# Kernel optimization log

Hardware: AMD Instinct MI355X
Metric: run time of the kernel (lower is better)

The kernel has to match this reference:

```python
import jax, jax.numpy as jnp
import numpy as np

F_IN = 512
F_OUT = 512
HEADS = 8  # all heads share the same weights in the original module
NEG_SLOPE = 0.01  # nn.LeakyReLU default
MASK_VAL = -1.0e10


def setup_inputs() -> dict:
    key = jax.random.key(0)
    ks = jax.random.split(key, 6)
    B, N = 8, 2048
    X_input = jax.random.normal(ks[0], (B, N, F_IN), dtype=jnp.float32)
    u = jax.random.uniform(ks[1], (B, N, N), dtype=jnp.float32)
    A_input = jnp.maximum((u < 0.02).astype(jnp.float32), jnp.eye(N, dtype=jnp.float32)[None])
    # learned params (nn.Linear stores W as [out,in]; we use [in,out] with x @ W)
    Wk = jax.random.normal(ks[2], (F_IN, F_OUT), dtype=jnp.float32) / np.sqrt(F_IN).astype(np.float32)
    bk = jnp.zeros((F_OUT,), dtype=jnp.float32)
    ws = jax.random.normal(ks[3], (F_OUT,), dtype=jnp.float32) / np.sqrt(F_OUT).astype(np.float32)
    bs = jnp.zeros((), dtype=jnp.float32)
    wn = jax.random.normal(ks[4], (F_OUT,), dtype=jnp.float32) / np.sqrt(F_OUT).astype(np.float32)
    bn = jnp.zeros((), dtype=jnp.float32)
    return {"X_input": X_input, "A_input": A_input, "Wk": Wk, "bk": bk,
            "ws": ws, "bs": bs, "wn": wn, "bn": bn}


def reference(X_input, A_input, Wk, bk, ws, bs, wn, bn):
    # shared projection (identical across all heads in the original loop)
    feat = jnp.einsum('bnf,fg->bng', X_input, Wk) + bk          # [B,N,F_]
    a_self = jnp.einsum('bng,g->bn', feat, ws) + bs             # [B,N]
    a_neigh = jnp.einsum('bng,g->bn', feat, wn) + bn            # [B,N]
    # torch.bmm([B,N,1],[B,1,N]) -> multiplicative outer product score
    att = jax.nn.leaky_relu(a_self[:, :, None] * a_neigh[:, None, :], NEG_SLOPE)
    att = att + MASK_VAL * (1.0 - A_input)                      # [B,N,N]
    p = jax.nn.softmax(att, axis=-1)
    nf = jnp.einsum('bij,bjg->big', p, feat)                    # [B,N,F_]
    # concat of HEADS identical head outputs, then tanh
    out = jnp.tanh(jnp.concatenate([nf] * HEADS, axis=-1))      # [B,N,HEADS*F_]
    return out
```

## Files before the change

kernel.cpp:

```cpp
#include <hip/hip_runtime.h>

#define NEG_SLOPE 0.01f
#define B_ 8
#define N_ 2048
#define F_ 512

typedef unsigned short u16;
typedef __attribute__((ext_vector_type(8))) unsigned short u16x8;
typedef __attribute__((ext_vector_type(8))) _Float16 f16x8;
typedef __attribute__((ext_vector_type(4))) float f32x4;

__device__ __forceinline__ f32x4 mfma16f(u16x8 a, u16x8 b, f32x4 c) {
    return __builtin_amdgcn_mfma_f32_16x16x32_f16(
        __builtin_bit_cast(f16x8, a), __builtin_bit_cast(f16x8, b), c, 0, 0, 0);
}

__device__ __forceinline__ void load_lds16(const void* g, void* l) {
    __builtin_amdgcn_global_load_lds(
        (__attribute__((address_space(1))) void*)(void*)g,
        (__attribute__((address_space(3))) void*)l, 16, 0, 0);
}

__global__ __launch_bounds__(256) void prep_all(const float* __restrict__ Wk,
                                                const float* __restrict__ bk,
                                                const float* __restrict__ ws,
                                                const float* __restrict__ bs,
                                                const float* __restrict__ wn,
                                                const float* __restrict__ bn,
                                                u16* __restrict__ Wf,
                                                float* __restrict__ ws2,
                                                float* __restrict__ wn2,
                                                float* __restrict__ csn) {
    const int bid = blockIdx.x, t = threadIdx.x;
    if (bid < 1024) {
        const int id = bid * 256 + t;
        const int k = id & 511, n = id >> 9;
        ((_Float16*)Wf)[id] = (_Float16)Wk[k * 512 + n];
        return;
    }
    const int lane = t & 63, w = t >> 6;
    if (bid >= 1280) {
        if (w == 0) {
            const int sel = bid - 1280;
            const float* vec = sel ? wn : ws;
            const float4 b0 = *(const float4*)(bk + lane * 8);
            const float4 b1 = *(const float4*)(bk + lane * 8 + 4);
            const float4 v0 = *(const float4*)(vec + lane * 8);
            const float4 v1 = *(const float4*)(vec + lane * 8 + 4);
            float d = b0.x * v0.x + b0.y * v0.y + b0.z * v0.z + b0.w * v0.w +
                      b1.x * v1.x + b1.y * v1.y + b1.z * v1.z + b1.w * v1.w;
#pragma unroll
            for (int m = 32; m; m >>= 1) d += __shfl_xor(d, m);
            if (lane == 0) csn[sel] = d + (sel ? bn[0] : bs[0]);
        }
        return;
    }
    const int W = (bid - 1024) * 4 + w;
    const int k = W & 511;
    const float* vec = (W < 512) ? ws : wn;
    const float4 w0 = *(const float4*)(Wk + (size_t)k * 512 + lane * 8);
    const float4 w1 = *(const float4*)(Wk + (size_t)k * 512 + lane * 8 + 4);
    const float4 v0 = *(const float4*)(vec + lane * 8);
    const float4 v1 = *(const float4*)(vec + lane * 8 + 4);
    float d = w0.x * v0.x + w0.y * v0.y + w0.z * v0.z + w0.w * v0.w +
              w1.x * v1.x + w1.y * v1.y + w1.z * v1.z + w1.w * v1.w;
#pragma unroll
    for (int m = 32; m; m >>= 1) d += __shfl_xor(d, m);
    if (lane == 0) ((W < 512) ? ws2 : wn2)[k] = d;
}

__global__ __launch_bounds__(256) void gemm_feat(const float* __restrict__ X,
                                                 const u16* __restrict__ Wf,
                                                 const float* __restrict__ bk,
                                                 u16* __restrict__ feat) {
    __shared__ u16 Af[128 * 64];
    __shared__ u16 Bf[128 * 64];
    const int t = threadIdx.x;
    const int lane = t & 63;
    const int w = t >> 6;
    const int bid = blockIdx.x;
    const int tm = (bid & 7) * 16 + (bid >> 5);
    const int tn = (bid >> 3) & 3;
    const int wr = w >> 1, wc = w & 1;

    f32x4 acc[4][4];
#pragma unroll
    for (int m = 0; m < 4; ++m)
#pragma unroll
        for (int n = 0; n < 4; ++n) acc[m][n] = {0.f, 0.f, 0.f, 0.f};

    const int lrow = lane >> 3;
    const int scol = ((lane & 7) ^ lrow) * 8;
    const u16* Bbase = Wf + ((size_t)(tn * 128 + w * 8 + lrow)) * 512 + scol;
    u16* BfW = Bf + (w * 8) * 64;

    const int arow = t >> 3;
    const int akk = (t & 7) * 8;
    const float* Abase = X + ((size_t)(tm * 128 + arow)) * 512 + akk;
    u16* AfW = Af + arow * 64 + (akk ^ ((arow & 7) * 8));

    for (int k0 = 0; k0 < 512; k0 += 64) {
#pragma unroll
        for (int iss = 0; iss < 4; ++iss)
            load_lds16(Bbase + (size_t)(iss * 32) * 512 + k0, BfW + iss * 32 * 64);
#pragma unroll
        for (int p = 0; p < 4; ++p) {
            const float4 x0 = *(const float4*)(Abase + (size_t)(p * 32) * 512 + k0);
            const float4 x1 = *(const float4*)(Abase + (size_t)(p * 32) * 512 + k0 + 4);
            const float xv[8] = {x0.x, x0.y, x0.z, x0.w, x1.x, x1.y, x1.z, x1.w};
            u16x8 hv;
#pragma unroll
            for (int e = 0; e < 8; ++e)
                hv[e] = __builtin_bit_cast(u16, (_Float16)xv[e]);
            *(u16x8*)(AfW + p * 32 * 64) = hv;
        }
        __syncthreads();
        const int swz = (lane & 7) * 8;
#pragma unroll
        for (int kk = 0; kk < 64; kk += 32) {
            u16x8 af[4], bf[4];
            const int aoff = (kk + (lane >> 4) * 8) ^ swz;
#pragma unroll
            for (int m = 0; m < 4; ++m)
                af[m] = *(const u16x8*)(Af + (wr * 64 + m * 16 + (lane & 15)) * 64 + aoff);
#pragma unroll
            for (int n = 0; n < 4; ++n)
                bf[n] = *(const u16x8*)(Bf + (wc * 64 + n * 16 + (lane & 15)) * 64 + aoff);
#pragma unroll
            for (int m = 0; m < 4; ++m)
#pragma unroll
                for (int n = 0; n < 4; ++n)
                    acc[m][n] = mfma16f(af[m], bf[n], acc[m][n]);
        }
        __syncthreads();
    }

    const int crow0 = tm * 128 + wr * 64;
    const int ccol0 = tn * 128 + wc * 64;
    _Float16* feat16 = (_Float16*)feat;
#pragma unroll
    for (int n = 0; n < 4; ++n) {
        const int gc = ccol0 + n * 16 + (lane & 15);
        const float bkv = bk[gc];
#pragma unroll
        for (int m = 0; m < 4; ++m) {
            const int gr = crow0 + m * 16 + (lane >> 4) * 4;
#pragma unroll
            for (int r = 0; r < 4; ++r)
                feat16[(size_t)(gr + r) * 512 + gc] = (_Float16)(acc[m][n][r] + bkv);
        }
    }
}

__global__ __launch_bounds__(256) void dots_x(const float* __restrict__ X,
                                              const float* __restrict__ ws2,
                                              const float* __restrict__ wn2,
                                              const float* __restrict__ csn,
                                              float* __restrict__ a_self,
                                              float* __restrict__ a_neigh) {
    const int t = threadIdx.x, lane = t & 63, w = t >> 6;
    const int row = blockIdx.x * 4 + w;
    const float4 f0 = *(const float4*)(X + (size_t)row * 512 + lane * 8);
    const float4 f1 = *(const float4*)(X + (size_t)row * 512 + lane * 8 + 4);
    const float fv[8] = {f0.x, f0.y, f0.z, f0.w, f1.x, f1.y, f1.z, f1.w};
    const float4 sa = *(const float4*)(ws2 + lane * 8);
    const float4 sb = *(const float4*)(ws2 + lane * 8 + 4);
    const float4 na = *(const float4*)(wn2 + lane * 8);
    const float4 nb = *(const float4*)(wn2 + lane * 8 + 4);
    float ds = fv[0] * sa.x + fv[1] * sa.y + fv[2] * sa.z + fv[3] * sa.w +
               fv[4] * sb.x + fv[5] * sb.y + fv[6] * sb.z + fv[7] * sb.w;
    float dn = fv[0] * na.x + fv[1] * na.y + fv[2] * na.z + fv[3] * na.w +
               fv[4] * nb.x + fv[5] * nb.y + fv[6] * nb.z + fv[7] * nb.w;
#pragma unroll
    for (int m = 32; m; m >>= 1) {
        ds += __shfl_xor(ds, m);
        dn += __shfl_xor(dn, m);
    }
    if (lane == 0) {
        a_self[row] = ds + csn[0];
        a_neigh[row] = dn + csn[1];
    }
}

__global__ __launch_bounds__(256) void attn_row(const float* __restrict__ A,
                                                const u16* __restrict__ feat,
                                                const float* __restrict__ a_self,
                                                const float* __restrict__ a_neigh,
                                                float* __restrict__ out) {
    const int bid = blockIdx.x;
    const int row = (bid & 7) * N_ + (bid >> 3);
    const int b = bid & 7;
    const int t = threadIdx.x;
    const int lane = t & 63, w = t >> 6;

    __shared__ u16   lj[N_];
    __shared__ float lsv[N_];
    __shared__ int   wtot[4];
    __shared__ float wred[8];
    __shared__ float nfw[4][F_];

    const float asi = a_self[row];

    const float4* Arow = (const float4*)(A + (size_t)row * N_);
    const float4* An   = (const float4*)(a_neigh + b * N_);
    const float4 a0 = Arow[t * 2], a1 = Arow[t * 2 + 1];
    const float4 n0 = An[t * 2],   n1 = An[t * 2 + 1];
    const float av[8] = {a0.x, a0.y, a0.z, a0.w, a1.x, a1.y, a1.z, a1.w};
    const float nv[8] = {n0.x, n0.y, n0.z, n0.w, n1.x, n1.y, n1.z, n1.w};
    float sv[8];
    int cnt = 0;
    float mloc = -3.0e38f;
#pragma unroll
    for (int e = 0; e < 8; ++e) {
        float s = asi * nv[e];
        s = s > 0.f ? s : NEG_SLOPE * s;
        sv[e] = s;
        if (av[e] != 0.f) { ++cnt; mloc = fmaxf(mloc, s); }
    }
    int v = cnt;
#pragma unroll
    for (int off = 1; off < 64; off <<= 1) {
        const int u = __shfl_up(v, off);
        if (lane >= off) v += u;
    }
#pragma unroll
    for (int m = 32; m; m >>= 1) mloc = fmaxf(mloc, __shfl_xor(mloc, m));
    if (lane == 63) wtot[w] = v;
    if (lane == 0) wred[w] = mloc;
    __syncthreads();
    int base = v - cnt;
#pragma unroll
    for (int i = 0; i < 4; ++i) base += (i < w) ? wtot[i] : 0;
    const int total = wtot[0] + wtot[1] + wtot[2] + wtot[3];
    const float mx = fmaxf(fmaxf(wred[0], wred[1]), fmaxf(wred[2], wred[3]));

    float ssum = 0.f;
    int pos = base;
#pragma unroll
    for (int e = 0; e < 8; ++e) {
        if (av[e] != 0.f) {
            const float wv = __expf(sv[e] - mx);
            lj[pos] = (u16)(t * 8 + e);
            lsv[pos] = wv;
            ssum += wv;
            ++pos;
        }
    }
#pragma unroll
    for (int m = 32; m; m >>= 1) ssum += __shfl_xor(ssum, m);
    if (lane == 0) wred[4 + w] = ssum;
    __syncthreads();
    const float inv = 1.f / (wred[4] + wred[5] + wred[6] + wred[7]);

    const u16* frow = feat + (size_t)b * N_ * F_ + lane * 8;
    float acc[8] = {0.f, 0.f, 0.f, 0.f, 0.f, 0.f, 0.f, 0.f};
    int k = w;
    for (; k + 4 < total; k += 8) {
        const size_t j0 = (size_t)lj[k] * F_, j1 = (size_t)lj[k + 4] * F_;
        const float p0 = lsv[k], p1 = lsv[k + 4];
        const f16x8 v0 = *(const f16x8*)(frow + j0);
        const f16x8 v1 = *(const f16x8*)(frow + j1);
#pragma unroll
        for (int e = 0; e < 8; ++e) acc[e] += p0 * (float)v0[e] + p1 * (float)v1[e];
    }
    if (k < total) {
        const size_t j0 = (size_t)lj[k] * F_;
        const float p0 = lsv[k];
        const f16x8 v0 = *(const f16x8*)(frow + j0);
#pragma unroll
        for (int e = 0; e < 8; ++e) acc[e] += p0 * (float)v0[e];
    }
#pragma unroll
    for (int e = 0; e < 8; ++e) nfw[w][lane * 8 + e] = acc[e];
    __syncthreads();

    const int f0 = t * 2;
    const float nf0 = (nfw[0][f0] + nfw[1][f0]) + (nfw[2][f0] + nfw[3][f0]);
    const float nf1 = (nfw[0][f0 + 1] + nfw[1][f0 + 1]) + (nfw[2][f0 + 1] + nfw[3][f0 + 1]);
    const float o0 = tanhf(nf0 * inv);
    const float o1 = tanhf(nf1 * inv);
    const float2 o = make_float2(o0, o1);
    float* obase = out + (size_t)row * (8 * F_) + f0;
#pragma unroll
    for (int h = 0; h < 8; ++h) *(float2*)(obase + h * F_) = o;
}

extern "C" void kernel_launch(void* const* d_in, const int* in_sizes, int n_in,
                              void* d_out, int out_size, void* d_ws, size_t ws_size,
                              hipStream_t stream) {
    const float* X  = (const float*)d_in[0];
    const float* A  = (const float*)d_in[1];
    const float* Wk = (const float*)d_in[2];
    const float* bk = (const float*)d_in[3];
    const float* ws = (const float*)d_in[4];
    const float* bs = (const float*)d_in[5];
    const float* wn = (const float*)d_in[6];
    const float* bn = (const float*)d_in[7];
    float* out = (float*)d_out;

    char* wsb = (char*)d_ws;
    u16*   feat    = (u16*)(wsb);
    u16*   Wf      = (u16*)(wsb + 16777216);
    float* a_self  = (float*)(wsb + 17301504);
    float* a_neigh = (float*)(wsb + 17367040);
    float* ws2     = (float*)(wsb + 17432576);
    float* wn2     = (float*)(wsb + 17434624);
    float* csn     = (float*)(wsb + 17436672);

    prep_all   <<<dim3(1282),  dim3(256), 0, stream>>>(Wk, bk, ws, bs, wn, bn, Wf, ws2, wn2, csn);
    gemm_feat  <<<dim3(512),   dim3(256), 0, stream>>>(X, Wf, bk, feat);
    dots_x     <<<dim3(4096),  dim3(256), 0, stream>>>(X, ws2, wn2, csn, a_self, a_neigh);
    attn_row   <<<dim3(16384), dim3(256), 0, stream>>>(A, feat, a_self, a_neigh, out);
}
```

Measured before the change: 146.2 us.

## Process one attention row per wavefront using ballot-driven sparse gather

Restructures attn_row so each 64-lane wave owns a whole row instead of a 256-thread block splitting one row. The nonzero adjacency entries are tracked in per-lane bitmasks, then walked with ballot/ctz while scores are broadcast by shuffle. This drops the LDS compaction, prefix scan, cross-wave reductions and all __syncthreads, and the grid shrinks to a quarter of the blocks. The cost is that the gather over neighbors is now serial within one wave, with no two-way unrolling and more exp evaluations per lane. It also swaps the launch order of dots_x and gemm_feat, which are independent.

```diff
diff --git a/kernel.cpp b/kernel.cpp
--- a/kernel.cpp
+++ b/kernel.cpp
@@ -188,101 +188,70 @@
                                                 const float* __restrict__ a_neigh,
                                                 float* __restrict__ out) {
     const int bid = blockIdx.x;
-    const int row = (bid & 7) * N_ + (bid >> 3);
-    const int b = bid & 7;
     const int t = threadIdx.x;
     const int lane = t & 63, w = t >> 6;
-
-    __shared__ u16   lj[N_];
-    __shared__ float lsv[N_];
-    __shared__ int   wtot[4];
-    __shared__ float wred[8];
-    __shared__ float nfw[4][F_];
+    const int b = bid & 7;
+    const int row = b * N_ + (bid >> 3) * 4 + w;
 
     const float asi = a_self[row];
-
-    const float4* Arow = (const float4*)(A + (size_t)row * N_);
-    const float4* An   = (const float4*)(a_neigh + b * N_);
-    const float4 a0 = Arow[t * 2], a1 = Arow[t * 2 + 1];
-    const float4 n0 = An[t * 2],   n1 = An[t * 2 + 1];
-    const float av[8] = {a0.x, a0.y, a0.z, a0.w, a1.x, a1.y, a1.z, a1.w};
-    const float nv[8] = {n0.x, n0.y, n0.z, n0.w, n1.x, n1.y, n1.z, n1.w};
-    float sv[8];
-    int cnt = 0;
+    const float4* Arow4 = (const float4*)(A + (size_t)row * N_);
+    const float4* An4   = (const float4*)(a_neigh + (size_t)b * N_);
+
+    float sv[32];
+    unsigned selbits = 0;
     float mloc = -3.0e38f;
 #pragma unroll
-    for (int e = 0; e < 8; ++e) {
-        float s = asi * nv[e];
-        s = s > 0.f ? s : NEG_SLOPE * s;
-        sv[e] = s;
-        if (av[e] != 0.f) { ++cnt; mloc = fmaxf(mloc, s); }
-    }
-    int v = cnt;
-#pragma unroll
-    for (int off = 1; off < 64; off <<= 1) {
-        const int u = __shfl_up(v, off);
-        if (lane >= off) v += u;
-    }
-#pragma unroll
-    for (int m = 32; m; m >>= 1) mloc = fmaxf(mloc, __shfl_xor(mloc, m));
-    if (lane == 63) wtot[w] = v;
-    if (lane == 0) wred[w] = mloc;
-    __syncthreads();
-    int base = v - cnt;
-#pragma unroll
-    for (int i = 0; i < 4; ++i) base += (i < w) ? wtot[i] : 0;
-    const int total = wtot[0] + wtot[1] + wtot[2] + wtot[3];
-    const float mx = fmaxf(fmaxf(wred[0], wred[1]), fmaxf(wred[2], wred[3]));
-
-    float ssum = 0.f;
-    int pos = base;
-#pragma unroll
-    for (int e = 0; e < 8; ++e) {
-        if (av[e] != 0.f) {
-            const float wv = __expf(sv[e] - mx);
-            lj[pos] = (u16)(t * 8 + e);
-            lsv[pos] = wv;
-            ssum += wv;
-            ++pos;
-        }
-    }
-#pragma unroll
-    for (int m = 32; m; m >>= 1) ssum += __shfl_xor(ssum, m);
-    if (lane == 0) wred[4 + w] = ssum;
-    __syncthreads();
-    const float inv = 1.f / (wred[4] + wred[5] + wred[6] + wred[7]);
+    for (int c = 0; c < 8; ++c) {
+        const float4 a  = Arow4[c * 64 + lane];
+        const float4 an = An4[c * 64 + lane];
+        const float avi[4] = {a.x, a.y, a.z, a.w};
+        const float ani[4] = {an.x, an.y, an.z, an.w};
+#pragma unroll
+        for (int i = 0; i < 4; ++i) {
+            float s = asi * ani[i];
+            s = s > 0.f ? s : NEG_SLOPE * s;
+            sv[c * 4 + i] = s;
+            if (avi[i] != 0.f) {
+                selbits |= 1u << (c * 4 + i);
+                mloc = fmaxf(mloc, s);
+            }
+        }
+    }
+    float mx = mloc;
+#pragma unroll
+    for (int m = 32; m; m >>= 1) mx = fmaxf(mx, __shfl_xor(mx, m));
 
     const u16* frow = feat + (size_t)b * N_ * F_ + lane * 8;
     float acc[8] = {0.f, 0.f, 0.f, 0.f, 0.f, 0.f, 0.f, 0.f};
-    int k = w;
-    for (; k + 4 < total; k += 8) {
-        const size_t j0 = (size_t)lj[k] * F_, j1 = (size_t)lj[k + 4] * F_;
-        const float p0 = lsv[k], p1 = lsv[k + 4];
-        const f16x8 v0 = *(const f16x8*)(frow + j0);
-        const f16x8 v1 = *(const f16x8*)(frow + j1);
-#pragma unroll
-        for (int e = 0; e < 8; ++e) acc[e] += p0 * (float)v0[e] + p1 * (float)v1[e];
-    }
-    if (k < total) {
-        const size_t j0 = (size_t)lj[k] * F_;
-        const float p0 = lsv[k];
-        const f16x8 v0 = *(const f16x8*)(frow + j0);
-#pragma unroll
-        for (int e = 0; e < 8; ++e) acc[e] += p0 * (float)v0[e];
-    }
-#pragma unroll
-    for (int e = 0; e < 8; ++e) nfw[w][lane * 8 + e] = acc[e];
-    __syncthreads();
-
-    const int f0 = t * 2;
-    const float nf0 = (nfw[0][f0] + nfw[1][f0]) + (nfw[2][f0] + nfw[3][f0]);
-    const float nf1 = (nfw[0][f0 + 1] + nfw[1][f0 + 1]) + (nfw[2][f0 + 1] + nfw[3][f0 + 1]);
-    const float o0 = tanhf(nf0 * inv);
-    const float o1 = tanhf(nf1 * inv);
-    const float2 o = make_float2(o0, o1);
-    float* obase = out + (size_t)row * (8 * F_) + f0;
-#pragma unroll
-    for (int h = 0; h < 8; ++h) *(float2*)(obase + h * F_) = o;
+    float ssum = 0.f;
+#pragma unroll
+    for (int e = 0; e < 32; ++e) {
+        unsigned long long mask = __ballot((selbits >> e) & 1u);
+        while (mask) {
+            const int l = __builtin_ctzll(mask);
+            mask &= mask - 1;
+            const float s = __shfl(sv[e], l);
+            const float p = __expf(s - mx);
+            const int j = (e >> 2) * 256 + l * 4 + (e & 3);
+            const f16x8 vv = *(const f16x8*)(frow + (size_t)j * F_);
+#pragma unroll
+            for (int i = 0; i < 8; ++i) acc[i] += p * (float)vv[i];
+            ssum += p;
+        }
+    }
+    const float inv = 1.f / ssum;
+
+    float o[8];
+#pragma unroll
+    for (int i = 0; i < 8; ++i) o[i] = tanhf(acc[i] * inv);
+    const float4 o0 = {o[0], o[1], o[2], o[3]};
+    const float4 o1 = {o[4], o[5], o[6], o[7]};
+    float* obase = out + (size_t)row * (8 * F_) + lane * 8;
+#pragma unroll
+    for (int h = 0; h < 8; ++h) {
+        *(float4*)(obase + h * F_)     = o0;
+        *(float4*)(obase + h * F_ + 4) = o1;
+    }
 }
 
 extern "C" void kernel_launch(void* const* d_in, const int* in_sizes, int n_in,
@@ -308,7 +277,7 @@
     float* csn     = (float*)(wsb + 17436672);
 
     prep_all   <<<dim3(1282),  dim3(256), 0, stream>>>(Wk, bk, ws, bs, wn, bn, Wf, ws2, wn2, csn);
+    dots_x     <<<dim3(4096),  dim3(256), 0, stream>>>(X, ws2, wn2, csn, a_self, a_neigh);
     gemm_feat  <<<dim3(512),   dim3(256), 0, stream>>>(X, Wf, bk, feat);
-    dots_x     <<<dim3(4096),  dim3(256), 0, stream>>>(X, ws2, wn2, csn, a_self, a_neigh);
-    attn_row   <<<dim3(16384), dim3(256), 0, stream>>>(A, feat, a_self, a_neigh, out);
-}
+    attn_row   <<<dim3(4096),  dim3(256), 0, stream>>>(A, feat, a_self, a_neigh, out);
+}
```

Result: slower. 160.5 us (+9.8%).
